# Performance work log

Measured on AMD Instinct MI355X. Metric: run time of the kernel, lower is better.

Reference implementation:

```python
import jax, jax.numpy as jnp
import numpy as np

EPS = 1e-5

def _ln(x, g, b):
    m = jnp.mean(x, axis=-1, keepdims=True)
    v = jnp.var(x, axis=-1, keepdims=True)
    return (x - m) * jax.lax.rsqrt(v + EPS) * g + b

def setup_inputs() -> dict:
    key = jax.random.key(0)
    ks = jax.random.split(key, 8)
    B, N, C, H = 2, 2048, 128, 8
    hid = 768
    s = lambda k, shp, fan: jax.random.normal(k, shp, jnp.float32) * (1.0 / np.sqrt(fan))
    return {
        "x1": jax.random.normal(ks[0], (B, N, C), jnp.float32),
        "x2": jax.random.normal(ks[1], (B, N, C), jnp.float32),
        "x3": jax.random.normal(ks[2], (B, N, C), jnp.float32),
        "ln1_g": jnp.ones((3, C), jnp.float32),
        "ln1_b": jnp.zeros((3, C), jnp.float32),
        "qkv_w": s(ks[3], (3, C, 3 * C), C),      # [branch, in, out]; torch Linear weight transposed
        "proj_w": s(ks[4], (3, C, C), C),
        "proj_b": jnp.zeros((3, C), jnp.float32),
        "ln2_g": jnp.ones((3 * C,), jnp.float32),
        "ln2_b": jnp.zeros((3 * C,), jnp.float32),
        "fc1_w": s(ks[5], (3 * C, hid), 3 * C),
        "fc1_b": jnp.zeros((hid,), jnp.float32),
        "fc2_w": s(ks[6], (hid, 3 * C), hid),
        "fc2_b": jnp.zeros((3 * C,), jnp.float32),
    }

def _branch(x, g, b, w_qkv, w_p, b_p, num_heads=8):
    B, N, C = x.shape
    hd = C // num_heads
    scale = hd ** -0.5
    xn = _ln(x, g, b)
    qkv = (xn @ w_qkv).reshape(B, N, 3, num_heads, hd)
    qkv = jnp.transpose(qkv, (2, 0, 3, 1, 4))  # [3,B,H,N,hd]
    q, k, v = qkv[0], qkv[1], qkv[2]
    attn = jax.nn.softmax(jnp.einsum('bhnd,bhmd->bhnm', q, k) * scale, axis=-1)
    o = jnp.einsum('bhnm,bhmd->bhnd', attn, v)
    o = jnp.transpose(o, (0, 2, 1, 3)).reshape(B, N, C)
    return x + (o @ w_p + b_p)

def reference(x1, x2, x3, ln1_g, ln1_b, qkv_w, proj_w, proj_b,
              ln2_g, ln2_b, fc1_w, fc1_b, fc2_w, fc2_b):
    xs = jnp.stack([x1, x2, x3])  # [3,B,N,C]
    xs = jax.vmap(_branch)(xs, ln1_g, ln1_b, qkv_w, proj_w, proj_b)
    B, N, C = x1.shape
    xc = jnp.transpose(xs, (1, 2, 0, 3)).reshape(B, N, 3 * C)  # concat(x1,x2,x3) on features
    h = jax.nn.gelu(_ln(xc, ln2_g, ln2_b) @ fc1_w + fc1_b, approximate=False)
    xc = xc + (h @ fc2_w + fc2_b)
    return xc[:, :, :C], xc[:, :, C:2 * C], xc[:, :, 2 * C:]
```

## Files before the change

kernel.cpp:

```cpp
#include <hip/hip_runtime.h>
#include <hip/hip_bf16.h>

typedef __hip_bfloat16 bf16;


static __device__ __forceinline__ float b2f(bf16 h) { return __bfloat162float(h); }
static __device__ __forceinline__ bf16 f2b(float f) { return __float2bfloat16(f); }
static __device__ __forceinline__ unsigned short f2bu(float f) {
    bf16 h = f2b(f);
    return *reinterpret_cast<unsigned short*>(&h);
}
static __device__ __forceinline__ float bs2f(short s) {
    return __uint_as_float(((unsigned)(unsigned short)s) << 16);
}

typedef __attribute__((ext_vector_type(8))) short short8;
typedef __attribute__((ext_vector_type(4))) short short4v;
typedef __attribute__((ext_vector_type(16))) float f32x16;
typedef __attribute__((ext_vector_type(2))) int int2v;

#define QSCALE 0.36067376022224085f

static __device__ __forceinline__ float xhalf(float x, int hi) {
    auto r = __builtin_amdgcn_permlane32_swap(__float_as_int(x), __float_as_int(x), false, false);
    return __int_as_float(hi ? r[0] : r[1]);
}

__global__ __launch_bounds__(256) void k_wt_all(const float* __restrict__ qkv_w, const float* __restrict__ proj_w,
                                                const float* __restrict__ fc1_w, const float* __restrict__ fc2_w,
                                                bf16* __restrict__ wtq, bf16* __restrict__ wtp,
                                                bf16* __restrict__ wt1, bf16* __restrict__ wt2) {
    int idx = blockIdx.x * 256 + threadIdx.x;
    if (idx < 147456) {
        int b = idx / 49152, i2 = idx % 49152;
        int n = i2 >> 7, k = i2 & 127;
        wtq[idx] = f2b(qkv_w[b * 49152 + k * 384 + n]);
    } else if (idx < 196608) {
        int j = idx - 147456;
        int b = j / 16384, i2 = j % 16384;
        int n = i2 >> 7, k = i2 & 127;
        wtp[j] = f2b(proj_w[b * 16384 + k * 128 + n]);
    } else if (idx < 491520) {
        int j = idx - 196608;
        int n = j / 384, k = j - n * 384;
        wt1[j] = f2b(fc1_w[k * 768 + n]);
    } else {
        int j = idx - 491520;
        int n = j / 768, k = j - n * 768;
        wt2[j] = f2b(fc2_w[k * 384 + n]);
    }
}

__device__ __forceinline__ f32x16 gemm_tile(const short* __restrict__ A, const short* __restrict__ W,
                                            int K, int rowbase, int colbase,
                                            short* als, short* wls) {
    int tid = threadIdx.x;
    int wid = tid >> 6, lane = tid & 63;
    int hi = lane >> 5, l31 = lane & 31;
    int wm = wid >> 1, wn = wid & 1;
    int sr = tid >> 3, skb = tid & 7;
    f32x16 acc;
#pragma unroll
    for (int i = 0; i < 16; ++i) acc[i] = 0.f;
    for (int k0 = 0; k0 < K; k0 += 64) {
        __syncthreads();
#pragma unroll
        for (int pass = 0; pass < 2; ++pass) {
            int r = sr + pass * 32;
            short8 av = *(const short8*)&A[(size_t)(rowbase + r) * K + k0 + skb * 8];
            *(short8*)&als[r * 64 + ((skb ^ (r & 7)) * 8)] = av;
            short8 wv = *(const short8*)&W[(size_t)(colbase + r) * K + k0 + skb * 8];
            *(short8*)&wls[r * 64 + ((skb ^ (r & 7)) * 8)] = wv;
        }
        __syncthreads();
#pragma unroll
        for (int ks = 0; ks < 4; ++ks) {
            int ra = wm * 32 + l31;
            int rb = wn * 32 + l31;
            int kb = ks * 2 + hi;
            short8 af = *(const short8*)&als[ra * 64 + ((kb ^ (ra & 7)) * 8)];
            short8 bf = *(const short8*)&wls[rb * 64 + ((kb ^ (rb & 7)) * 8)];
            acc = __builtin_amdgcn_mfma_f32_32x32x16_bf16(af, bf, acc, 0, 0, 0);
        }
    }
    return acc;
}

__global__ __launch_bounds__(256) void k_ln1(const float* __restrict__ x1, const float* __restrict__ x2,
                                             const float* __restrict__ x3, const float* __restrict__ g,
                                             const float* __restrict__ b, bf16* __restrict__ xn) {
    int tid = threadIdx.x;
    int wave = tid >> 6, lane = tid & 63;
    int grow = blockIdx.x * 4 + wave;
    int branch = grow >> 12;
    const float* xp = (branch == 0) ? x1 : (branch == 1 ? x2 : x3);
    const float* row = xp + (size_t)(grow & 4095) * 128;
    float2 a = *reinterpret_cast<const float2*>(&row[2 * lane]);
    float s = a.x + a.y, sq = a.x * a.x + a.y * a.y;
#pragma unroll
    for (int off = 32; off >= 1; off >>= 1) { s += __shfl_xor(s, off); sq += __shfl_xor(sq, off); }
    float mean = s * (1.f / 128.f);
    float var = sq * (1.f / 128.f) - mean * mean;
    float rstd = rsqrtf(var + 1e-5f);
    float2 gv = *reinterpret_cast<const float2*>(&g[branch * 128 + 2 * lane]);
    float2 bv = *reinterpret_cast<const float2*>(&b[branch * 128 + 2 * lane]);
    bf16* orow = xn + (size_t)grow * 128;
    orow[2 * lane] = f2b((a.x - mean) * rstd * gv.x + bv.x);
    orow[2 * lane + 1] = f2b((a.y - mean) * rstd * gv.y + bv.y);
}

__global__ __launch_bounds__(256) void k_qkv_m(const bf16* __restrict__ xn, const bf16* __restrict__ wt,
                                               bf16* __restrict__ q, bf16* __restrict__ k, bf16* __restrict__ v) {
    __shared__ short als[64 * 64];
    __shared__ short wls[64 * 64];
    int branch = blockIdx.z;
    const short* A = (const short*)xn + (size_t)branch * 4096 * 128;
    const short* W = (const short*)wt + (size_t)branch * 384 * 128;
    int rowbase = blockIdx.x * 64, colbase = blockIdx.y * 64;
    f32x16 acc = gemm_tile(A, W, 128, rowbase, colbase, als, wls);
    int tid = threadIdx.x, wid = tid >> 6, lane = tid & 63;
    int hi = lane >> 5, l31 = lane & 31;
    int wm = wid >> 1, wn = wid & 1;
    int c = colbase + wn * 32 + l31;
    int which = c >> 7, h = (c >> 4) & 7, d = c & 15;
    bf16* dst = (which == 0) ? q : (which == 1 ? k : v);
    float scl = (which == 0) ? QSCALE : 1.0f;
#pragma unroll
    for (int i = 0; i < 16; ++i) {
        int mrow = (i & 3) + 8 * (i >> 2) + 4 * hi;
        int token = rowbase + wm * 32 + mrow;
        int bb = token >> 11, n = token & 2047;
        dst[((((size_t)branch * 2 + bb) * 8 + h) * 2048 + n) * 16 + d] = f2b(acc[i] * scl);
    }
}

__global__ __launch_bounds__(128, 4) void k_attn(const bf16* __restrict__ qg, const bf16* __restrict__ kg,
                                                 const bf16* __restrict__ vg, bf16* __restrict__ pacc,
                                                 float2* __restrict__ psm) {
    __shared__ short vt[2][16 * 64];
    int bh = blockIdx.x;
    int qblk = blockIdx.y;
    int split = blockIdx.z;
    size_t base = (size_t)bh * (2048 * 16);
    int tid = threadIdx.x, wave = tid >> 6, lane = tid & 63;
    int hi = lane >> 5, l31 = lane & 31;
    int qrow = qblk * 64 + wave * 32 + l31;
    const short* qs = (const short*)qg;
    const short* ks = (const short*)kg;
    const short* vs = (const short*)vg;
    short8 qf = *(const short8*)&qs[base + (size_t)qrow * 16 + hi * 8];

    f32x16 acc;
    f32x16 negm;
#pragma unroll
    for (int r = 0; r < 16; ++r) { acc[r] = 0.f; negm[r] = -16.f; }
    float m = 16.f, sum = 0.f;

    int sd = tid & 15, sk0 = (tid >> 4) * 8;
    int swzs = (sd & 7) << 3;
    int kbeg = split * 1024, kend = kbeg + 1024;

    {
        short va[8];
#pragma unroll
        for (int j = 0; j < 8; ++j) va[j] = vs[base + (size_t)(kbeg + sk0 + j) * 16 + sd];
        short8 wv;
#pragma unroll
        for (int j = 0; j < 8; ++j) wv[j] = va[j];
        *(short8*)&vt[0][sd * 64 + (sk0 ^ swzs)] = wv;
    }
    __syncthreads();

    for (int c0 = kbeg; c0 < kend; c0 += 64) {
        int cur = (c0 >> 6) & 1;
        bool more = (c0 + 64) < kend;
        short8 kf0 = *(const short8*)&ks[base + (size_t)(c0 + l31) * 16 + hi * 8];
        short8 kf1 = *(const short8*)&ks[base + (size_t)(c0 + 32 + l31) * 16 + hi * 8];
        short va[8];
        if (more) {
#pragma unroll
            for (int j = 0; j < 8; ++j) va[j] = vs[base + (size_t)(c0 + 64 + sk0 + j) * 16 + sd];
        }
        f32x16 pa = __builtin_amdgcn_mfma_f32_32x32x16_bf16(kf0, qf, negm, 0, 0, 0);
        f32x16 pb = __builtin_amdgcn_mfma_f32_32x32x16_bf16(kf1, qf, negm, 0, 0, 0);
#pragma unroll
        for (int r = 0; r < 16; ++r) pa[r] = __builtin_amdgcn_exp2f(pa[r]);
#pragma unroll
        for (int r = 0; r < 16; ++r) pb[r] = __builtin_amdgcn_exp2f(pb[r]);
        float e0 = 0.f, e1 = 0.f, e2 = 0.f, e3 = 0.f;
#pragma unroll
        for (int r = 0; r < 16; r += 4) { e0 += pa[r]; e1 += pa[r + 1]; e2 += pa[r + 2]; e3 += pa[r + 3]; }
#pragma unroll
        for (int r = 0; r < 16; r += 4) { e0 += pb[r]; e1 += pb[r + 1]; e2 += pb[r + 2]; e3 += pb[r + 3]; }
        float psum = (e0 + e1) + (e2 + e3);
        if (__any(psum > 256.f)) {
            float p0 = fmaxf(pa[0], pa[1]), p1 = fmaxf(pa[2], pa[3]);
#pragma unroll
            for (int r = 4; r < 16; r += 4) { p0 = fmaxf(p0, fmaxf(pa[r], pa[r + 1])); p1 = fmaxf(p1, fmaxf(pa[r + 2], pa[r + 3])); }
#pragma unroll
            for (int r = 0; r < 16; r += 4) { p0 = fmaxf(p0, fmaxf(pb[r], pb[r + 1])); p1 = fmaxf(p1, fmaxf(pb[r + 2], pb[r + 3])); }
            float pmax = fmaxf(p0, p1);
            pmax = fmaxf(pmax, xhalf(pmax, hi));
            float delta = fmaxf(0.f, __log2f(pmax));
            float fac = __builtin_amdgcn_exp2f(-delta);
            m += delta;
#pragma unroll
            for (int r = 0; r < 16; ++r) negm[r] = -m;
            sum *= fac; psum *= fac;
#pragma unroll
            for (int r = 0; r < 16; ++r) { pa[r] *= fac; pb[r] *= fac; acc[r] *= fac; }
        }
        sum += psum;
        unsigned wa[8], wb[8];
#pragma unroll
        for (int e = 0; e < 8; ++e) {
            unsigned t;
            asm("v_cvt_pk_bf16_f32 %0, %1, %2" : "=v"(t) : "v"(pa[2 * e]), "v"(pa[2 * e + 1]));
            wa[e] = t;
            asm("v_cvt_pk_bf16_f32 %0, %1, %2" : "=v"(t) : "v"(pb[2 * e]), "v"(pb[2 * e + 1]));
            wb[e] = t;
        }
        union { unsigned u[4]; short8 v; } b1, b2, b3, b4;
        {
            auto r0 = __builtin_amdgcn_permlane32_swap((int)wa[0], (int)wa[2], false, false);
            b1.u[0] = (unsigned)r0[0]; b1.u[2] = (unsigned)r0[1];
            auto r1 = __builtin_amdgcn_permlane32_swap((int)wa[1], (int)wa[3], false, false);
            b1.u[1] = (unsigned)r1[0]; b1.u[3] = (unsigned)r1[1];
            auto r2 = __builtin_amdgcn_permlane32_swap((int)wa[4], (int)wa[6], false, false);
            b2.u[0] = (unsigned)r2[0]; b2.u[2] = (unsigned)r2[1];
            auto r3 = __builtin_amdgcn_permlane32_swap((int)wa[5], (int)wa[7], false, false);
            b2.u[1] = (unsigned)r3[0]; b2.u[3] = (unsigned)r3[1];
            auto r4 = __builtin_amdgcn_permlane32_swap((int)wb[0], (int)wb[2], false, false);
            b3.u[0] = (unsigned)r4[0]; b3.u[2] = (unsigned)r4[1];
            auto r5 = __builtin_amdgcn_permlane32_swap((int)wb[1], (int)wb[3], false, false);
            b3.u[1] = (unsigned)r5[0]; b3.u[3] = (unsigned)r5[1];
            auto r6 = __builtin_amdgcn_permlane32_swap((int)wb[4], (int)wb[6], false, false);
            b4.u[0] = (unsigned)r6[0]; b4.u[2] = (unsigned)r6[1];
            auto r7 = __builtin_amdgcn_permlane32_swap((int)wb[5], (int)wb[7], false, false);
            b4.u[1] = (unsigned)r7[0]; b4.u[3] = (unsigned)r7[1];
        }
        int d = lane & 15;
        short8 vf;
        vf = *(const short8*)&vt[cur][(d * 64 + hi * 8) ^ ((d & 7) << 3)];
        acc = __builtin_amdgcn_mfma_f32_32x32x16_bf16(vf, b1.v, acc, 0, 0, 0);
        vf = *(const short8*)&vt[cur][(d * 64 + 16 + hi * 8) ^ ((d & 7) << 3)];
        acc = __builtin_amdgcn_mfma_f32_32x32x16_bf16(vf, b2.v, acc, 0, 0, 0);
        vf = *(const short8*)&vt[cur][(d * 64 + 32 + hi * 8) ^ ((d & 7) << 3)];
        acc = __builtin_amdgcn_mfma_f32_32x32x16_bf16(vf, b3.v, acc, 0, 0, 0);
        vf = *(const short8*)&vt[cur][(d * 64 + 48 + hi * 8) ^ ((d & 7) << 3)];
        acc = __builtin_amdgcn_mfma_f32_32x32x16_bf16(vf, b4.v, acc, 0, 0, 0);
        if (more) {
            short8 wv;
#pragma unroll
            for (int j = 0; j < 8; ++j) wv[j] = va[j];
            *(short8*)&vt[cur ^ 1][sd * 64 + (sk0 ^ swzs)] = wv;
        }
        __syncthreads();
    }
    float sumt = sum + xhalf(sum, hi);
    size_t pidx = ((size_t)(split * 48 + bh) * 2048 + qrow) * 16;
    unsigned u0 = (unsigned)f2bu(acc[0]) | ((unsigned)f2bu(acc[1]) << 16);
    unsigned u1 = (unsigned)f2bu(acc[2]) | ((unsigned)f2bu(acc[3]) << 16);
    unsigned u2 = (unsigned)f2bu(acc[4]) | ((unsigned)f2bu(acc[5]) << 16);
    unsigned u3 = (unsigned)f2bu(acc[6]) | ((unsigned)f2bu(acc[7]) << 16);
    short* pp = (short*)pacc;
    int2v w01; w01.x = (int)u0; w01.y = (int)u1;
    int2v w23; w23.x = (int)u2; w23.y = (int)u3;
    *(int2v*)&pp[pidx + 4 * hi] = w01;
    *(int2v*)&pp[pidx + 8 + 4 * hi] = w23;
    if (hi == 0) {
        float2 sm; sm.x = sumt; sm.y = m;
        psm[(size_t)(split * 48 + bh) * 2048 + qrow] = sm;
    }
}

__global__ __launch_bounds__(256) void k_attn_red(const bf16* __restrict__ pacc, const float2* __restrict__ psm,
                                                  bf16* __restrict__ o) {
    int t = blockIdx.x * 256 + threadIdx.x;
    int hi = t & 1;
    int qrow = (t >> 1) & 2047;
    int bh = t >> 12;
    size_t ridx = (size_t)bh * 2048 + qrow;
    float2 sm0 = psm[ridx];
    float2 sm1 = psm[(size_t)48 * 2048 + ridx];
    float mp = fmaxf(sm0.y, sm1.y);
    float w0 = __builtin_amdgcn_exp2f(sm0.y - mp);
    float w1 = __builtin_amdgcn_exp2f(sm1.y - mp);
    float inv = 1.f / (sm0.x * w0 + sm1.x * w1);
    w0 *= inv; w1 *= inv;
    const short* p0 = (const short*)pacc + ridx * 16;
    const short* p1 = (const short*)pacc + (size_t)48 * 2048 * 16 + ridx * 16;
    short4v a0 = *(const short4v*)&p0[4 * hi];
    short4v c0 = *(const short4v*)&p0[8 + 4 * hi];
    short4v a1 = *(const short4v*)&p1[4 * hi];
    short4v c1 = *(const short4v*)&p1[8 + 4 * hi];
    unsigned u0, u1, u2, u3;
    {
        float f0 = bs2f(a0[0]) * w0 + bs2f(a1[0]) * w1;
        float f1 = bs2f(a0[1]) * w0 + bs2f(a1[1]) * w1;
        float f2 = bs2f(a0[2]) * w0 + bs2f(a1[2]) * w1;
        float f3 = bs2f(a0[3]) * w0 + bs2f(a1[3]) * w1;
        u0 = (unsigned)f2bu(f0) | ((unsigned)f2bu(f1) << 16);
        u1 = (unsigned)f2bu(f2) | ((unsigned)f2bu(f3) << 16);
        float g0 = bs2f(c0[0]) * w0 + bs2f(c1[0]) * w1;
        float g1 = bs2f(c0[1]) * w0 + bs2f(c1[1]) * w1;
        float g2 = bs2f(c0[2]) * w0 + bs2f(c1[2]) * w1;
        float g3 = bs2f(c0[3]) * w0 + bs2f(c1[3]) * w1;
        u2 = (unsigned)f2bu(g0) | ((unsigned)f2bu(g1) << 16);
        u3 = (unsigned)f2bu(g2) | ((unsigned)f2bu(g3) << 16);
    }
    int branch = bh >> 4, bb = (bh >> 3) & 1, h = bh & 7;
    size_t orow = (size_t)branch * 4096 + (size_t)bb * 2048 + qrow;
    short* op = (short*)o;
    int2v w01; w01.x = (int)u0; w01.y = (int)u1;
    int2v w23; w23.x = (int)u2; w23.y = (int)u3;
    *(int2v*)&op[orow * 128 + h * 16 + 4 * hi] = w01;
    *(int2v*)&op[orow * 128 + h * 16 + 8 + 4 * hi] = w23;
}

__global__ __launch_bounds__(256) void k_proj_m(const bf16* __restrict__ ob, const bf16* __restrict__ wt,
                                                const float* __restrict__ pb, const float* __restrict__ x1,
                                                const float* __restrict__ x2, const float* __restrict__ x3,
                                                float* __restrict__ xc) {
    __shared__ short als[64 * 64];
    __shared__ short wls[64 * 64];
    int branch = blockIdx.z;
    const short* A = (const short*)ob + (size_t)branch * 4096 * 128;
    const short* W = (const short*)wt + (size_t)branch * 128 * 128;
    int rowbase = blockIdx.x * 64, colbase = blockIdx.y * 64;
    f32x16 acc = gemm_tile(A, W, 128, rowbase, colbase, als, wls);
    int tid = threadIdx.x, wid = tid >> 6, lane = tid & 63;
    int hi = lane >> 5, l31 = lane & 31;
    int wm = wid >> 1, wn = wid & 1;
    int c = colbase + wn * 32 + l31;
    float bias = pb[branch * 128 + c];
    const float* xp = (branch == 0) ? x1 : (branch == 1 ? x2 : x3);
#pragma unroll
    for (int i = 0; i < 16; ++i) {
        int mrow = (i & 3) + 8 * (i >> 2) + 4 * hi;
        int row = rowbase + wm * 32 + mrow;
        xc[(size_t)row * 384 + branch * 128 + c] = acc[i] + bias + xp[(size_t)row * 128 + c];
    }
}

__global__ __launch_bounds__(256) void k_ln2(const float* __restrict__ xc, const float* __restrict__ g,
                                             const float* __restrict__ b, bf16* __restrict__ xcn) {
    int tid = threadIdx.x, wave = tid >> 6, lane = tid & 63;
    int row = blockIdx.x * 4 + wave;
    const float* rp = xc + (size_t)row * 384;
    float v[6];
    float s = 0.f, sq = 0.f;
#pragma unroll
    for (int i = 0; i < 6; ++i) {
        v[i] = rp[lane + i * 64];
        s += v[i]; sq += v[i] * v[i];
    }
#pragma unroll
    for (int off = 32; off >= 1; off >>= 1) { s += __shfl_xor(s, off); sq += __shfl_xor(sq, off); }
    float mean = s * (1.f / 384.f);
    float var = sq * (1.f / 384.f) - mean * mean;
    float rstd = rsqrtf(var + 1e-5f);
    bf16* op = xcn + (size_t)row * 384;
#pragma unroll
    for (int i = 0; i < 6; ++i) {
        int c = lane + i * 64;
        op[c] = f2b((v[i] - mean) * rstd * g[c] + b[c]);
    }
}

__global__ __launch_bounds__(256) void k_fc1_m(const bf16* __restrict__ xcn, const bf16* __restrict__ wt,
                                               const float* __restrict__ bias, bf16* __restrict__ h) {
    __shared__ short als[64 * 64];
    __shared__ short wls[64 * 64];
    const short* A = (const short*)xcn;
    const short* W = (const short*)wt;
    int rowbase = blockIdx.x * 64, colbase = blockIdx.y * 64;
    f32x16 acc = gemm_tile(A, W, 384, rowbase, colbase, als, wls);
    int tid = threadIdx.x, wid = tid >> 6, lane = tid & 63;
    int hi = lane >> 5, l31 = lane & 31;
    int wm = wid >> 1, wn = wid & 1;
    int c = colbase + wn * 32 + l31;
    float bs = bias[c];
#pragma unroll
    for (int i = 0; i < 16; ++i) {
        int mrow = (i & 3) + 8 * (i >> 2) + 4 * hi;
        int row = rowbase + wm * 32 + mrow;
        float vv = acc[i] + bs;
        float ge = 0.5f * vv * (1.f + erff(vv * 0.70710678118f));
        h[(size_t)row * 768 + c] = f2b(ge);
    }
}

__global__ __launch_bounds__(256) void k_fc2_m(const bf16* __restrict__ h, const bf16* __restrict__ wt,
                                               const float* __restrict__ bias, const float* __restrict__ xc,
                                               float* __restrict__ outp) {
    __shared__ short als[64 * 64];
    __shared__ short wls[64 * 64];
    const short* A = (const short*)h;
    const short* W = (const short*)wt;
    int rowbase = blockIdx.x * 64, colbase = blockIdx.y * 64;
    f32x16 acc = gemm_tile(A, W, 768, rowbase, colbase, als, wls);
    int tid = threadIdx.x, wid = tid >> 6, lane = tid & 63;
    int hi = lane >> 5, l31 = lane & 31;
    int wm = wid >> 1, wn = wid & 1;
    int c = colbase + wn * 32 + l31;
    float bs = bias[c];
    int which = c >> 7, cc = c & 127;
#pragma unroll
    for (int i = 0; i < 16; ++i) {
        int mrow = (i & 3) + 8 * (i >> 2) + 4 * hi;
        int row = rowbase + wm * 32 + mrow;
        outp[(size_t)which * 524288 + (size_t)row * 128 + cc] = acc[i] + bs + xc[(size_t)row * 384 + c];
    }
}

extern "C" void kernel_launch(void* const* d_in, const int* in_sizes, int n_in,
                              void* d_out, int out_size, void* d_ws, size_t ws_size,
                              hipStream_t stream) {
    const float* x1     = (const float*)d_in[0];
    const float* x2     = (const float*)d_in[1];
    const float* x3     = (const float*)d_in[2];
    const float* ln1_g  = (const float*)d_in[3];
    const float* ln1_b  = (const float*)d_in[4];
    const float* qkv_w  = (const float*)d_in[5];
    const float* proj_w = (const float*)d_in[6];
    const float* proj_b = (const float*)d_in[7];
    const float* ln2_g  = (const float*)d_in[8];
    const float* ln2_b  = (const float*)d_in[9];
    const float* fc1_w  = (const float*)d_in[10];
    const float* fc1_b  = (const float*)d_in[11];
    const float* fc2_w  = (const float*)d_in[12];
    const float* fc2_b  = (const float*)d_in[13];

    char* ws = (char*)d_ws;
    const size_t SB = 3145728;
    bf16* xn  = (bf16*)(ws + 0 * SB);
    bf16* qb  = (bf16*)(ws + 1 * SB);
    bf16* kb  = (bf16*)(ws + 2 * SB);
    bf16* vb  = (bf16*)(ws + 3 * SB);
    bf16* ob  = (bf16*)(ws + 4 * SB);
    float* xc = (float*)(ws + 5 * SB);
    bf16* xcn = (bf16*)(ws + 5 * SB + 6291456);
    bf16* hb  = (bf16*)(ws + 6 * SB + 6291456);
    char* wbase = ws + 31457280;
    bf16* wtq = (bf16*)(wbase);
    bf16* wtp = (bf16*)(wbase + 294912);
    bf16* wt1 = (bf16*)(wbase + 393216);
    bf16* wt2 = (bf16*)(wbase + 983040);
    bf16*  pacc = (bf16*)(ws + 22020096);
    float2* psm = (float2*)(ws + 28311552);

    k_wt_all<<<3072, 256, 0, stream>>>(qkv_w, proj_w, fc1_w, fc2_w, wtq, wtp, wt1, wt2);
    k_ln1<<<3072, 256, 0, stream>>>(x1, x2, x3, ln1_g, ln1_b, xn);
    k_qkv_m<<<dim3(64, 6, 3), 256, 0, stream>>>(xn, wtq, qb, kb, vb);
    k_attn<<<dim3(48, 32, 2), 128, 0, stream>>>(qb, kb, vb, pacc, psm);
    k_attn_red<<<768, 256, 0, stream>>>(pacc, psm, ob);
    k_proj_m<<<dim3(64, 2, 3), 256, 0, stream>>>(ob, wtp, proj_b, x1, x2, x3, xc);
    k_ln2<<<1024, 256, 0, stream>>>(xc, ln2_g, ln2_b, xcn);
    k_fc1_m<<<dim3(64, 12, 1), 256, 0, stream>>>(xcn, wt1, fc1_b, hb);
    k_fc2_m<<<dim3(64, 6, 1), 256, 0, stream>>>(hb, wt2, fc2_b, xc, (float*)d_out);
}
```

Baseline: 104.4 us.

## Store V transposed from QKV GEMM and load V fragments directly in attention

The QKV projection now writes V in a [branch,b,h,d,n] transposed layout, so the attention kernel can load its V MFMA operands straight from global memory as contiguous 8-element vectors. This removes the shared-memory double buffer, the scalar strided V loads, the LDS transpose and the per-iteration __syncthreads. In exchange, the V store in the GEMM epilogue becomes strided along the token dimension, and each wave reads V from global or L2 memory itself instead of sharing a staged copy with the other wave in its block.

```diff
diff --git a/kernel.cpp b/kernel.cpp
--- a/kernel.cpp
+++ b/kernel.cpp
@@ -123,32 +123,44 @@
     int wm = wid >> 1, wn = wid & 1;
     int c = colbase + wn * 32 + l31;
     int which = c >> 7, h = (c >> 4) & 7, d = c & 15;
-    bf16* dst = (which == 0) ? q : (which == 1 ? k : v);
-    float scl = (which == 0) ? QSCALE : 1.0f;
-#pragma unroll
-    for (int i = 0; i < 16; ++i) {
-        int mrow = (i & 3) + 8 * (i >> 2) + 4 * hi;
-        int token = rowbase + wm * 32 + mrow;
-        int bb = token >> 11, n = token & 2047;
-        dst[((((size_t)branch * 2 + bb) * 8 + h) * 2048 + n) * 16 + d] = f2b(acc[i] * scl);
+    if (which < 2) {
+        bf16* dst = (which == 0) ? q : k;
+        float scl = (which == 0) ? QSCALE : 1.0f;
+#pragma unroll
+        for (int i = 0; i < 16; ++i) {
+            int mrow = (i & 3) + 8 * (i >> 2) + 4 * hi;
+            int token = rowbase + wm * 32 + mrow;
+            int bb = token >> 11, n = token & 2047;
+            dst[((((size_t)branch * 2 + bb) * 8 + h) * 2048 + n) * 16 + d] = f2b(acc[i] * scl);
+        }
+    } else {
+#pragma unroll
+        for (int i = 0; i < 16; ++i) {
+            int mrow = (i & 3) + 8 * (i >> 2) + 4 * hi;
+            int token = rowbase + wm * 32 + mrow;
+            int bb = token >> 11, n = token & 2047;
+            v[((((size_t)branch * 2 + bb) * 8 + h) * 16 + d) * 2048 + n] = f2b(acc[i]);
+        }
     }
 }
 
 __global__ __launch_bounds__(128, 4) void k_attn(const bf16* __restrict__ qg, const bf16* __restrict__ kg,
                                                  const bf16* __restrict__ vg, bf16* __restrict__ pacc,
                                                  float2* __restrict__ psm) {
-    __shared__ short vt[2][16 * 64];
     int bh = blockIdx.x;
     int qblk = blockIdx.y;
     int split = blockIdx.z;
     size_t base = (size_t)bh * (2048 * 16);
+    size_t baset = (size_t)bh * (16 * 2048);
     int tid = threadIdx.x, wave = tid >> 6, lane = tid & 63;
     int hi = lane >> 5, l31 = lane & 31;
     int qrow = qblk * 64 + wave * 32 + l31;
     const short* qs = (const short*)qg;
     const short* ks = (const short*)kg;
-    const short* vs = (const short*)vg;
+    const short* vts = (const short*)vg;
     short8 qf = *(const short8*)&qs[base + (size_t)qrow * 16 + hi * 8];
+    int d = lane & 15;
+    const short* vrow = &vts[baset + (size_t)d * 2048 + hi * 8];
 
     f32x16 acc;
     f32x16 negm;
@@ -156,31 +168,15 @@
     for (int r = 0; r < 16; ++r) { acc[r] = 0.f; negm[r] = -16.f; }
     float m = 16.f, sum = 0.f;
 
-    int sd = tid & 15, sk0 = (tid >> 4) * 8;
-    int swzs = (sd & 7) << 3;
     int kbeg = split * 1024, kend = kbeg + 1024;
 
-    {
-        short va[8];
-#pragma unroll
-        for (int j = 0; j < 8; ++j) va[j] = vs[base + (size_t)(kbeg + sk0 + j) * 16 + sd];
-        short8 wv;
-#pragma unroll
-        for (int j = 0; j < 8; ++j) wv[j] = va[j];
-        *(short8*)&vt[0][sd * 64 + (sk0 ^ swzs)] = wv;
-    }
-    __syncthreads();
-
     for (int c0 = kbeg; c0 < kend; c0 += 64) {
-        int cur = (c0 >> 6) & 1;
-        bool more = (c0 + 64) < kend;
         short8 kf0 = *(const short8*)&ks[base + (size_t)(c0 + l31) * 16 + hi * 8];
         short8 kf1 = *(const short8*)&ks[base + (size_t)(c0 + 32 + l31) * 16 + hi * 8];
-        short va[8];
-        if (more) {
-#pragma unroll
-            for (int j = 0; j < 8; ++j) va[j] = vs[base + (size_t)(c0 + 64 + sk0 + j) * 16 + sd];
-        }
+        short8 vf1 = *(const short8*)&vrow[c0];
+        short8 vf2 = *(const short8*)&vrow[c0 + 16];
+        short8 vf3 = *(const short8*)&vrow[c0 + 32];
+        short8 vf4 = *(const short8*)&vrow[c0 + 48];
         f32x16 pa = __builtin_amdgcn_mfma_f32_32x32x16_bf16(kf0, qf, negm, 0, 0, 0);
         f32x16 pb = __builtin_amdgcn_mfma_f32_32x32x16_bf16(kf1, qf, negm, 0, 0, 0);
 #pragma unroll
@@ -239,23 +235,10 @@
             auto r7 = __builtin_amdgcn_permlane32_swap((int)wb[5], (int)wb[7], false, false);
             b4.u[1] = (unsigned)r7[0]; b4.u[3] = (unsigned)r7[1];
         }
-        int d = lane & 15;
-        short8 vf;
-        vf = *(const short8*)&vt[cur][(d * 64 + hi * 8) ^ ((d & 7) << 3)];
-        acc = __builtin_amdgcn_mfma_f32_32x32x16_bf16(vf, b1.v, acc, 0, 0, 0);
-        vf = *(const short8*)&vt[cur][(d * 64 + 16 + hi * 8) ^ ((d & 7) << 3)];
-        acc = __builtin_amdgcn_mfma_f32_32x32x16_bf16(vf, b2.v, acc, 0, 0, 0);
-        vf = *(const short8*)&vt[cur][(d * 64 + 32 + hi * 8) ^ ((d & 7) << 3)];
-        acc = __builtin_amdgcn_mfma_f32_32x32x16_bf16(vf, b3.v, acc, 0, 0, 0);
-        vf = *(const short8*)&vt[cur][(d * 64 + 48 + hi * 8) ^ ((d & 7) << 3)];
-        acc = __builtin_amdgcn_mfma_f32_32x32x16_bf16(vf, b4.v, acc, 0, 0, 0);
-        if (more) {
-            short8 wv;
-#pragma unroll
-            for (int j = 0; j < 8; ++j) wv[j] = va[j];
-            *(short8*)&vt[cur ^ 1][sd * 64 + (sk0 ^ swzs)] = wv;
-        }
-        __syncthreads();
+        acc = __builtin_amdgcn_mfma_f32_32x32x16_bf16(vf1, b1.v, acc, 0, 0, 0);
+        acc = __builtin_amdgcn_mfma_f32_32x32x16_bf16(vf2, b2.v, acc, 0, 0, 0);
+        acc = __builtin_amdgcn_mfma_f32_32x32x16_bf16(vf3, b3.v, acc, 0, 0, 0);
+        acc = __builtin_amdgcn_mfma_f32_32x32x16_bf16(vf4, b4.v, acc, 0, 0, 0);
     }
     float sumt = sum + xhalf(sum, hi);
     size_t pidx = ((size_t)(split * 48 + bh) * 2048 + qrow) * 16;
```

New measurement: 119.6 us. 1.15x slower.
